# Optimization experiments

Hardware: AMD Instinct MI355X
Metric: run time of the kernel (lower is better)

Reference implementation:

```python
import jax, jax.numpy as jnp
import numpy as np

SYM_LIST = np.array([0, 2, 5], dtype=np.int64)


def quat_to_rot_wxyz(q):
    """q: [bs, 4] normalized quaternion in wxyz order -> [bs, 3, 3] rotation."""
    w, x, y, z = q[:, 0], q[:, 1], q[:, 2], q[:, 3]
    two = jnp.asarray(2.0, q.dtype)
    one = jnp.asarray(1.0, q.dtype)
    r00 = one - two * (y * y + z * z)
    r01 = two * (x * y - z * w)
    r02 = two * (x * z + y * w)
    r10 = two * (x * y + z * w)
    r11 = one - two * (x * x + z * z)
    r12 = two * (y * z - x * w)
    r20 = two * (x * z - y * w)
    r21 = two * (y * z + x * w)
    r22 = one - two * (x * x + y * y)
    R = jnp.stack([
        jnp.stack([r00, r01, r02], axis=-1),
        jnp.stack([r10, r11, r12], axis=-1),
        jnp.stack([r20, r21, r22], axis=-1),
    ], axis=-2)  # [bs, 3, 3]
    return R


def setup_inputs() -> dict:
    key = jax.random.key(0)
    k1, k2, k3, k4, k5 = jax.random.split(key, 5)
    bs, num_p = 32, 2048
    pred_r = jax.random.normal(k1, (bs, 4), dtype=jnp.float32)
    pred_t = jax.random.normal(k2, (bs, 3), dtype=jnp.float32)
    target = jax.random.normal(k3, (bs, num_p, 3), dtype=jnp.float32)
    model_points = jax.random.normal(k4, (bs, num_p, 3), dtype=jnp.float32)
    idx = jax.random.randint(k5, (bs, 1), 0, 8, dtype=jnp.int64)
    return {"pred_r": pred_r, "pred_t": pred_t, "target": target,
            "model_points": model_points, "idx": idx, "permutation": 0}


def reference(pred_r, pred_t, target, model_points, idx, permutation):
    # normalize quaternion, build rotation, transform model points (row-vector
    # convention as in torch.bmm(model_points, base))
    q = pred_r / jnp.linalg.norm(pred_r, axis=1, keepdims=True)  # [bs,4]
    R = quat_to_rot_wxyz(q)                                      # [bs,3,3]
    tf = jnp.einsum('bnd,bde->bne', model_points, R) + pred_t[:, None, :]  # [bs,N,3]

    # brute-force 1-NN: for each transformed model point, nearest target point
    # squared distances via the ||a||^2 + ||b||^2 - 2 a.b expansion: [bs,N,N]
    d2 = (jnp.sum(tf * tf, axis=-1)[:, :, None]
          + jnp.sum(target * target, axis=-1)[:, None, :]
          - 2.0 * jnp.einsum('bnd,bmd->bnm', tf, target))
    inds = jnp.argmin(d2, axis=-1)                               # [bs,N]
    matched = jnp.take_along_axis(target, inds[..., None], axis=1)  # [bs,N,3]

    # apply the symmetric (ADD-S) matching only for classes in sym_list
    sym_mask = jnp.isin(idx[:, 0], jnp.asarray(SYM_LIST))        # [bs]
    target2 = jnp.where(sym_mask[:, None, None], matched, target)

    dis = jnp.mean(jnp.linalg.norm(tf - target, axis=2), axis=1)    # ADD (returned)
    dis2 = jnp.mean(jnp.linalg.norm(tf - target2, axis=2), axis=1)  # ADD-S (knn-matched)
    return jnp.stack([dis, dis2])  # [2, bs]
```

## Files before the change

### kernel.cpp

```cpp
#include <hip/hip_runtime.h>
#include <math.h>

#define NP      2048
#define BS      32
#define TPB     1024
#define NW      (TPB / 64)
#define WSLICE  (NP / NW)
#define PPT     4
#define PTSBLK  (64 * PPT)
#define SLICES  (NP / PTSBLK)

__global__ __launch_bounds__(TPB, 4) void loss_fused_kernel(
    const float* __restrict__ pred_r,
    const float* __restrict__ pred_t,
    const float* __restrict__ target,
    const float* __restrict__ model_points,
    const int*   __restrict__ idx,
    float* __restrict__ out)
{
    __shared__ float4 tgt[NP];
    __shared__ float  pe[NW][PTSBLK];
    __shared__ int    pm[NW][PTSBLK];
    __shared__ float  red1[4], red2[4];

    const int b    = blockIdx.x >> 3;
    const int s    = blockIdx.x & 7;
    const int tid  = threadIdx.x;
    const int wave = tid >> 6;
    const int lane = tid & 63;

    float qw = pred_r[b * 4 + 0];
    float qx = pred_r[b * 4 + 1];
    float qy = pred_r[b * 4 + 2];
    float qz = pred_r[b * 4 + 3];
    float nrm = sqrtf(qw * qw + qx * qx + qy * qy + qz * qz);
    qw /= nrm; qx /= nrm; qy /= nrm; qz /= nrm;

    const float r00 = 1.0f - 2.0f * (qy * qy + qz * qz);
    const float r01 = 2.0f * (qx * qy - qz * qw);
    const float r02 = 2.0f * (qx * qz + qy * qw);
    const float r10 = 2.0f * (qx * qy + qz * qw);
    const float r11 = 1.0f - 2.0f * (qx * qx + qz * qz);
    const float r12 = 2.0f * (qy * qz - qx * qw);
    const float r20 = 2.0f * (qx * qz - qy * qw);
    const float r21 = 2.0f * (qy * qz + qx * qw);
    const float r22 = 1.0f - 2.0f * (qx * qx + qy * qy);

    const float tx = pred_t[b * 3 + 0];
    const float ty = pred_t[b * 3 + 1];
    const float tz = pred_t[b * 3 + 2];

    const float* tb = target + (size_t)b * NP * 3;
    #pragma unroll
    for (int k = 0; k < NP / TPB; ++k) {
        int j = tid + k * TPB;
        float t0 = tb[j * 3 + 0];
        float t1 = tb[j * 3 + 1];
        float t2 = tb[j * 3 + 2];
        tgt[j] = make_float4(t0, t1, t2, (t0 * t0 + t1 * t1) + t2 * t2);
    }

    float ax[PPT], ay[PPT], az[PPT], eb[PPT];
    int   mb[PPT];
    const float* mpb = model_points + (size_t)b * NP * 3;
    #pragma unroll
    for (int p = 0; p < PPT; ++p) {
        int n = s * PTSBLK + p * 64 + lane;
        float m0 = mpb[n * 3 + 0], m1 = mpb[n * 3 + 1], m2 = mpb[n * 3 + 2];
        float tfx = m0 * r00 + m1 * r10 + m2 * r20 + tx;
        float tfy = m0 * r01 + m1 * r11 + m2 * r21 + ty;
        float tfz = m0 * r02 + m1 * r12 + m2 * r22 + tz;
        ax[p] = -2.0f * tfx; ay[p] = -2.0f * tfy; az[p] = -2.0f * tfz;
        eb[p] = INFINITY;    mb[p] = 0;
    }
    __syncthreads();

    const int lc = wave * WSLICE;
    #pragma unroll 2
    for (int mm = 0; mm < WSLICE; mm += 4) {
        float4 c0 = tgt[lc + mm + 0];
        float4 c1 = tgt[lc + mm + 1];
        float4 c2 = tgt[lc + mm + 2];
        float4 c3 = tgt[lc + mm + 3];
        const int gm = lc + mm;
        #pragma unroll
        for (int p = 0; p < PPT; ++p) {
            float e0 = fmaf(ax[p], c0.x, fmaf(ay[p], c0.y, fmaf(az[p], c0.z, c0.w)));
            if (e0 < eb[p]) { eb[p] = e0; mb[p] = gm + 0; }
            float e1 = fmaf(ax[p], c1.x, fmaf(ay[p], c1.y, fmaf(az[p], c1.z, c1.w)));
            if (e1 < eb[p]) { eb[p] = e1; mb[p] = gm + 1; }
            float e2 = fmaf(ax[p], c2.x, fmaf(ay[p], c2.y, fmaf(az[p], c2.z, c2.w)));
            if (e2 < eb[p]) { eb[p] = e2; mb[p] = gm + 2; }
            float e3 = fmaf(ax[p], c3.x, fmaf(ay[p], c3.y, fmaf(az[p], c3.z, c3.w)));
            if (e3 < eb[p]) { eb[p] = e3; mb[p] = gm + 3; }
        }
    }

    #pragma unroll
    for (int p = 0; p < PPT; ++p) {
        pe[wave][p * 64 + lane] = eb[p];
        pm[wave][p * 64 + lane] = mb[p];
    }
    __syncthreads();

    float s1 = 0.0f, s2 = 0.0f;
    if (tid < PTSBLK) {
        float bE = pe[0][tid];
        int   bM = pm[0][tid];
        #pragma unroll
        for (int w = 1; w < NW; ++w) {
            float e = pe[w][tid];
            int   m = pm[w][tid];
            if (e < bE || (e == bE && m < bM)) { bE = e; bM = m; }
        }
        const int n = s * PTSBLK + tid;
        float m0 = mpb[n * 3 + 0], m1 = mpb[n * 3 + 1], m2 = mpb[n * 3 + 2];
        float tfx = m0 * r00 + m1 * r10 + m2 * r20 + tx;
        float tfy = m0 * r01 + m1 * r11 + m2 * r21 + ty;
        float tfz = m0 * r02 + m1 * r12 + m2 * r22 + tz;

        float4 tn = tgt[n];
        float dx = tfx - tn.x, dy = tfy - tn.y, dz = tfz - tn.z;
        float dis = sqrtf(dx * dx + dy * dy + dz * dz);
        float dis2 = dis;

        int iv = idx[b];
        bool sym = (iv == 0) | (iv == 2) | (iv == 5);
        if (sym) {
            float4 tm = tgt[bM];
            float sx = tfx - tm.x, sy = tfy - tm.y, sz = tfz - tm.z;
            dis2 = sqrtf(sx * sx + sy * sy + sz * sz);
        }
        s1 = dis; s2 = dis2;
    }

    #pragma unroll
    for (int off = 32; off > 0; off >>= 1) {
        s1 += __shfl_down(s1, off);
        s2 += __shfl_down(s2, off);
    }
    if (lane == 0 && wave < 4) { red1[wave] = s1; red2[wave] = s2; }
    __syncthreads();
    if (tid == 0) {
        float t1 = (red1[0] + red1[1]) + (red1[2] + red1[3]);
        float t2 = (red2[0] + red2[1]) + (red2[2] + red2[3]);
        atomicAdd(out + b,      t1 * (1.0f / NP));
        atomicAdd(out + 32 + b, t2 * (1.0f / NP));
    }
}

extern "C" void kernel_launch(void* const* d_in, const int* in_sizes, int n_in,
                              void* d_out, int out_size, void* d_ws, size_t ws_size,
                              hipStream_t stream) {
    const float* pred_r       = (const float*)d_in[0];
    const float* pred_t       = (const float*)d_in[1];
    const float* target       = (const float*)d_in[2];
    const float* model_points = (const float*)d_in[3];
    const int*   idx          = (const int*)d_in[4];
    float* out = (float*)d_out;

    loss_fused_kernel<<<BS * SLICES, TPB, 0, stream>>>(
        pred_r, pred_t, target, model_points, idx, out);
}
```

Measured before the change: 84.50 us.

## Skip nearest-neighbor search for non-symmetric classes and use packed-key tree reduction

Reads the class index first and runs the target staging and brute-force 1-NN scan only when the batch element's class is symmetric, since the matched index is otherwise unused. Non-symmetric blocks read their own target point straight from global memory. The cross-wave argmin now packs an order-preserving float bit pattern and the index into a 64-bit key, reduced in two 4-way stages instead of a serial 16-way compare loop. The skip depends on how many batch elements are symmetric, and the blocks now do uneven amounts of work.

Measured after the change: 82.05 us. 1.03x faster.

```diff
diff --git a/kernel.cpp b/kernel.cpp
--- a/kernel.cpp
+++ b/kernel.cpp
@@ -1,5 +1,6 @@
 #include <hip/hip_runtime.h>
 #include <math.h>
+#include <stdint.h>
 
 #define NP      2048
 #define BS      32
@@ -19,15 +20,18 @@
     float* __restrict__ out)
 {
     __shared__ float4 tgt[NP];
-    __shared__ float  pe[NW][PTSBLK];
-    __shared__ int    pm[NW][PTSBLK];
-    __shared__ float  red1[4], red2[4];
+    __shared__ unsigned long long key[NW][PTSBLK];
+    __shared__ unsigned long long key1[4][PTSBLK];
+    __shared__ float red1[4], red2[4];
 
     const int b    = blockIdx.x >> 3;
     const int s    = blockIdx.x & 7;
     const int tid  = threadIdx.x;
     const int wave = tid >> 6;
     const int lane = tid & 63;
+
+    const int iv   = idx[b];
+    const bool sym = (iv == 0) | (iv == 2) | (iv == 5);
 
     float qw = pred_r[b * 4 + 0];
     float qx = pred_r[b * 4 + 1];
@@ -50,82 +54,104 @@
     const float ty = pred_t[b * 3 + 1];
     const float tz = pred_t[b * 3 + 2];
 
-    const float* tb = target + (size_t)b * NP * 3;
-    #pragma unroll
-    for (int k = 0; k < NP / TPB; ++k) {
-        int j = tid + k * TPB;
-        float t0 = tb[j * 3 + 0];
-        float t1 = tb[j * 3 + 1];
-        float t2 = tb[j * 3 + 2];
-        tgt[j] = make_float4(t0, t1, t2, (t0 * t0 + t1 * t1) + t2 * t2);
-    }
+    const float* tb  = target + (size_t)b * NP * 3;
+    const float* mpb = model_points + (size_t)b * NP * 3;
 
-    float ax[PPT], ay[PPT], az[PPT], eb[PPT];
-    int   mb[PPT];
-    const float* mpb = model_points + (size_t)b * NP * 3;
-    #pragma unroll
-    for (int p = 0; p < PPT; ++p) {
-        int n = s * PTSBLK + p * 64 + lane;
-        float m0 = mpb[n * 3 + 0], m1 = mpb[n * 3 + 1], m2 = mpb[n * 3 + 2];
-        float tfx = m0 * r00 + m1 * r10 + m2 * r20 + tx;
-        float tfy = m0 * r01 + m1 * r11 + m2 * r21 + ty;
-        float tfz = m0 * r02 + m1 * r12 + m2 * r22 + tz;
-        ax[p] = -2.0f * tfx; ay[p] = -2.0f * tfy; az[p] = -2.0f * tfz;
-        eb[p] = INFINITY;    mb[p] = 0;
-    }
-    __syncthreads();
+    int bM = 0;
+    if (sym) {
+        #pragma unroll
+        for (int k = 0; k < NP / TPB; ++k) {
+            int j = tid + k * TPB;
+            float t0 = tb[j * 3 + 0];
+            float t1 = tb[j * 3 + 1];
+            float t2 = tb[j * 3 + 2];
+            tgt[j] = make_float4(t0, t1, t2, (t0 * t0 + t1 * t1) + t2 * t2);
+        }
 
-    const int lc = wave * WSLICE;
-    #pragma unroll 2
-    for (int mm = 0; mm < WSLICE; mm += 4) {
-        float4 c0 = tgt[lc + mm + 0];
-        float4 c1 = tgt[lc + mm + 1];
-        float4 c2 = tgt[lc + mm + 2];
-        float4 c3 = tgt[lc + mm + 3];
-        const int gm = lc + mm;
+        float ax[PPT], ay[PPT], az[PPT], eb[PPT];
+        int   mb[PPT];
         #pragma unroll
         for (int p = 0; p < PPT; ++p) {
-            float e0 = fmaf(ax[p], c0.x, fmaf(ay[p], c0.y, fmaf(az[p], c0.z, c0.w)));
-            if (e0 < eb[p]) { eb[p] = e0; mb[p] = gm + 0; }
-            float e1 = fmaf(ax[p], c1.x, fmaf(ay[p], c1.y, fmaf(az[p], c1.z, c1.w)));
-            if (e1 < eb[p]) { eb[p] = e1; mb[p] = gm + 1; }
-            float e2 = fmaf(ax[p], c2.x, fmaf(ay[p], c2.y, fmaf(az[p], c2.z, c2.w)));
-            if (e2 < eb[p]) { eb[p] = e2; mb[p] = gm + 2; }
-            float e3 = fmaf(ax[p], c3.x, fmaf(ay[p], c3.y, fmaf(az[p], c3.z, c3.w)));
-            if (e3 < eb[p]) { eb[p] = e3; mb[p] = gm + 3; }
+            int n = s * PTSBLK + p * 64 + lane;
+            float m0 = mpb[n * 3 + 0], m1 = mpb[n * 3 + 1], m2 = mpb[n * 3 + 2];
+            float tfx = m0 * r00 + m1 * r10 + m2 * r20 + tx;
+            float tfy = m0 * r01 + m1 * r11 + m2 * r21 + ty;
+            float tfz = m0 * r02 + m1 * r12 + m2 * r22 + tz;
+            ax[p] = -2.0f * tfx; ay[p] = -2.0f * tfy; az[p] = -2.0f * tfz;
+            eb[p] = INFINITY;    mb[p] = 0;
+        }
+        __syncthreads();
+
+        const int lc = wave * WSLICE;
+        #pragma unroll 2
+        for (int mm = 0; mm < WSLICE; mm += 4) {
+            float4 c0 = tgt[lc + mm + 0];
+            float4 c1 = tgt[lc + mm + 1];
+            float4 c2 = tgt[lc + mm + 2];
+            float4 c3 = tgt[lc + mm + 3];
+            const int gm = lc + mm;
+            #pragma unroll
+            for (int p = 0; p < PPT; ++p) {
+                float e0 = fmaf(ax[p], c0.x, fmaf(ay[p], c0.y, fmaf(az[p], c0.z, c0.w)));
+                if (e0 < eb[p]) { eb[p] = e0; mb[p] = gm + 0; }
+                float e1 = fmaf(ax[p], c1.x, fmaf(ay[p], c1.y, fmaf(az[p], c1.z, c1.w)));
+                if (e1 < eb[p]) { eb[p] = e1; mb[p] = gm + 1; }
+                float e2 = fmaf(ax[p], c2.x, fmaf(ay[p], c2.y, fmaf(az[p], c2.z, c2.w)));
+                if (e2 < eb[p]) { eb[p] = e2; mb[p] = gm + 2; }
+                float e3 = fmaf(ax[p], c3.x, fmaf(ay[p], c3.y, fmaf(az[p], c3.z, c3.w)));
+                if (e3 < eb[p]) { eb[p] = e3; mb[p] = gm + 3; }
+            }
+        }
+
+        #pragma unroll
+        for (int p = 0; p < PPT; ++p) {
+            float e = eb[p];
+            e = (e == 0.0f) ? 0.0f : e;
+            uint32_t u = __float_as_uint(e);
+            u ^= (uint32_t)((int32_t)u >> 31) | 0x80000000u;
+            key[wave][p * 64 + lane] =
+                ((unsigned long long)u << 32) | (uint32_t)mb[p];
+        }
+        __syncthreads();
+
+        {
+            int g = tid >> 8;
+            int p = tid & 255;
+            unsigned long long k0 = key[g * 4 + 0][p];
+            unsigned long long k1 = key[g * 4 + 1][p];
+            unsigned long long k2 = key[g * 4 + 2][p];
+            unsigned long long k3 = key[g * 4 + 3][p];
+            if (k1 < k0) k0 = k1;
+            if (k3 < k2) k2 = k3;
+            if (k2 < k0) k0 = k2;
+            key1[g][p] = k0;
+        }
+        __syncthreads();
+
+        if (tid < PTSBLK) {
+            unsigned long long k0 = key1[0][tid];
+            unsigned long long k1 = key1[1][tid];
+            unsigned long long k2 = key1[2][tid];
+            unsigned long long k3 = key1[3][tid];
+            if (k1 < k0) k0 = k1;
+            if (k3 < k2) k2 = k3;
+            if (k2 < k0) k0 = k2;
+            bM = (int)(uint32_t)k0;
         }
     }
 
-    #pragma unroll
-    for (int p = 0; p < PPT; ++p) {
-        pe[wave][p * 64 + lane] = eb[p];
-        pm[wave][p * 64 + lane] = mb[p];
-    }
-    __syncthreads();
-
     float s1 = 0.0f, s2 = 0.0f;
     if (tid < PTSBLK) {
-        float bE = pe[0][tid];
-        int   bM = pm[0][tid];
-        #pragma unroll
-        for (int w = 1; w < NW; ++w) {
-            float e = pe[w][tid];
-            int   m = pm[w][tid];
-            if (e < bE || (e == bE && m < bM)) { bE = e; bM = m; }
-        }
         const int n = s * PTSBLK + tid;
         float m0 = mpb[n * 3 + 0], m1 = mpb[n * 3 + 1], m2 = mpb[n * 3 + 2];
         float tfx = m0 * r00 + m1 * r10 + m2 * r20 + tx;
         float tfy = m0 * r01 + m1 * r11 + m2 * r21 + ty;
         float tfz = m0 * r02 + m1 * r12 + m2 * r22 + tz;
 
-        float4 tn = tgt[n];
-        float dx = tfx - tn.x, dy = tfy - tn.y, dz = tfz - tn.z;
+        float t0 = tb[n * 3 + 0], t1 = tb[n * 3 + 1], t2 = tb[n * 3 + 2];
+        float dx = tfx - t0, dy = tfy - t1, dz = tfz - t2;
         float dis = sqrtf(dx * dx + dy * dy + dz * dz);
         float dis2 = dis;
-
-        int iv = idx[b];
-        bool sym = (iv == 0) | (iv == 2) | (iv == 5);
         if (sym) {
             float4 tm = tgt[bM];
             float sx = tfx - tm.x, sy = tfy - tm.y, sz = tfz - tm.z;
```
